# Performance work log

Hardware: AMD Instinct MI355X
Metric: run time of the kernel (lower is better)

Reference implementation:

```python
import jax, jax.numpy as jnp
import numpy as np

# Gemma2-9B layer config
HID = 3584
H = 16          # query heads
KV = 8          # kv heads
G = H // KV     # GQA group size
DH = 256        # head dim
INTER = 14336
WINDOW = 1024   # sliding window size
LOGIT_CAP = 50.0
SCALING = 256.0 ** -0.5   # query_pre_attn_scalar ** -0.5
EPS = 1e-6
ROPE_BASE = 10000.0
B, S = 2, 2048


def gemma_rmsnorm(x, w, eps=EPS):
    # Gemma RMSNorm: fp32 compute, scale by (1 + w)
    xf = x.astype(jnp.float32)
    var = jnp.mean(xf * xf, axis=-1, keepdims=True)
    return (xf * jax.lax.rsqrt(var + eps) * (1.0 + w.astype(jnp.float32))).astype(x.dtype)


def apply_rope(pos, x):
    # neox-style rotary embedding; x: [B, S, n_heads, DH], pos: [B, S]
    half = DH // 2
    inv_freq = 1.0 / (ROPE_BASE ** (jnp.arange(0, half, dtype=jnp.float32) / half * 1.0))
    inv_freq = 1.0 / (ROPE_BASE ** (jnp.arange(0, DH, 2, dtype=jnp.float32) / DH))
    ang = pos.astype(jnp.float32)[..., None] * inv_freq          # [B, S, half]
    cos = jnp.cos(ang)[:, :, None, :]                            # [B, S, 1, half]
    sin = jnp.sin(ang)[:, :, None, :]
    x1, x2 = x[..., :half], x[..., half:]
    return jnp.concatenate([x1 * cos - x2 * sin, x2 * cos + x1 * sin], axis=-1).astype(x.dtype)


def setup_inputs() -> dict:
    key = jax.random.key(0)
    ks = jax.random.split(key, 12)
    s = 0.02
    inp = {
        "hidden_states": jax.random.normal(ks[0], (B, S, HID), dtype=jnp.float32),
        "positions": jnp.tile(jnp.arange(S, dtype=jnp.int32)[None, :], (B, 1)),
        "in_ln_w": jax.random.normal(ks[1], (HID,), dtype=jnp.float32) * s,
        "post_attn_ln_w": jax.random.normal(ks[2], (HID,), dtype=jnp.float32) * s,
        "pre_ff_ln_w": jax.random.normal(ks[3], (HID,), dtype=jnp.float32) * s,
        "post_ff_ln_w": jax.random.normal(ks[4], (HID,), dtype=jnp.float32) * s,
        "q_w": jax.random.normal(ks[5], (HID, H * DH), dtype=jnp.float32) * s,
        "k_w": jax.random.normal(ks[6], (HID, KV * DH), dtype=jnp.float32) * s,
        "v_w": jax.random.normal(ks[7], (HID, KV * DH), dtype=jnp.float32) * s,
        "o_w": jax.random.normal(ks[8], (H * DH, HID), dtype=jnp.float32) * s,
        "gate_w": jax.random.normal(ks[9], (HID, INTER), dtype=jnp.float32) * s,
        "up_w": jax.random.normal(ks[10], (HID, INTER), dtype=jnp.float32) * s,
        "down_w": jax.random.normal(ks[11], (INTER, HID), dtype=jnp.float32) * s,
    }
    return inp


def _decoder_layer(hidden_states, positions, in_ln_w, post_attn_ln_w, pre_ff_ln_w,
                   post_ff_ln_w, q_w, k_w, v_w, o_w, gate_w, up_w, down_w):
    # residual is None path
    residual = hidden_states
    x = gemma_rmsnorm(hidden_states, in_ln_w)

    # ---- attention ----
    q = (x @ q_w).reshape(B, S, H, DH)
    k = (x @ k_w).reshape(B, S, KV, DH)
    v = (x @ v_w).reshape(B, S, KV, DH)
    q = apply_rope(positions, q)
    k = apply_rope(positions, k)
    kv_fused = jnp.stack([k, v], axis=0)  # paged KV-cache write, modeled densely

    qg = q.reshape(B, S, KV, G, DH)
    # scores: [B, KV, G, S(q), S(k)]
    scores = jnp.einsum('bsngd,btnd->bngst', qg, k) * SCALING
    scores = LOGIT_CAP * jnp.tanh(scores / LOGIT_CAP)  # logit softcapping
    i = jnp.arange(S)[:, None]
    j = jnp.arange(S)[None, :]
    mask = (j <= i) & (i - j < WINDOW)                 # causal + sliding window
    scores = jnp.where(mask, scores, jnp.finfo(scores.dtype).min)
    probs = jax.nn.softmax(scores, axis=-1)
    attn = jnp.einsum('bngst,btnd->bsngd', probs, v).reshape(B, S, H * DH)
    attn_out = attn @ o_w

    x = gemma_rmsnorm(attn_out, post_attn_ln_w)
    x = residual + x
    residual = x

    # ---- GeGLU MLP ----
    x = gemma_rmsnorm(x, pre_ff_ln_w)
    inter = (x @ up_w) * jax.nn.gelu(x @ gate_w)
    x = inter @ down_w
    x = gemma_rmsnorm(x, post_ff_ln_w)
    return x, residual, kv_fused


def reference(hidden_states, positions, in_ln_w, post_attn_ln_w, pre_ff_ln_w,
              post_ff_ln_w, q_w, k_w, v_w, o_w, gate_w, up_w, down_w):
    return _decoder_layer(hidden_states, positions, in_ln_w, post_attn_ln_w,
                          pre_ff_ln_w, post_ff_ln_w, q_w, k_w, v_w, o_w,
                          gate_w, up_w, down_w)
```

## Files before the change

kernel.cpp:

```cpp
#include <hip/hip_runtime.h>
#include <stdint.h>

typedef unsigned short ushortT;
typedef float f32x4 __attribute__((ext_vector_type(4)));
typedef short short8 __attribute__((ext_vector_type(8)));

#define HID 3584
#define NH 16
#define NKV 8
#define DH 256
#define SEQ 2048
#define NB 2
#define NTOK 4096
#define INTERDIM 14336
#define ICH 7168
#define WINDOW 1024

__device__ __forceinline__ ushortT f2bf(float x) {
  union { float f; uint32_t u; } v; v.f = x;
  uint32_t r = v.u + 0x7fffu + ((v.u >> 16) & 1u);
  return (ushortT)(r >> 16);
}
__device__ __forceinline__ float bf2f(uint32_t b) {
  union { uint32_t u; float f; } v; v.u = b << 16;
  return v.f;
}
__device__ __forceinline__ void gll16(const void* g, void* l) {
  __builtin_amdgcn_global_load_lds((const __attribute__((address_space(1))) void*)g,
                                   (__attribute__((address_space(3))) void*)l, 16, 0, 0);
}
__device__ __forceinline__ void sbar() {
  asm volatile("" ::: "memory");
  __builtin_amdgcn_s_barrier();
  asm volatile("" ::: "memory");
}
__device__ __forceinline__ void vmdrain() {
  asm volatile("s_waitcnt vmcnt(0)" ::: "memory");
}

__global__ __launch_bounds__(256) void transpose_cvt(const float* __restrict__ in,
                                                     ushortT* __restrict__ out,
                                                     int in_rs, int out_rs) {
  __shared__ float tile[64][65];
  const int r0 = blockIdx.y * 64, c0 = blockIdx.x * 64;
  const int t = threadIdx.x, tc = (t & 15) * 4, tr = t >> 4;
#pragma unroll
  for (int p = 0; p < 4; ++p) {
    int r = tr + p * 16;
    float4 v = *(const float4*)&in[(size_t)(r0 + r) * in_rs + c0 + tc];
    tile[r][tc] = v.x; tile[r][tc + 1] = v.y; tile[r][tc + 2] = v.z; tile[r][tc + 3] = v.w;
  }
  __syncthreads();
#pragma unroll
  for (int p = 0; p < 4; ++p) {
    int r = tr + p * 16;
    ushort4 u;
    u.x = f2bf(tile[tc + 0][r]); u.y = f2bf(tile[tc + 1][r]);
    u.z = f2bf(tile[tc + 2][r]); u.w = f2bf(tile[tc + 3][r]);
    *(ushort4*)&out[(size_t)(c0 + r) * out_rs + r0 + tc] = u;
  }
}

__global__ __launch_bounds__(256) void vtrans(const float* __restrict__ vsrc,
                                              ushortT* __restrict__ vT) {
  __shared__ float tile[64][65];
  const int z = blockIdx.z, b = z >> 3, n = z & 7;
  const float* in = vsrc + (size_t)b * SEQ * (NKV * DH) + n * DH;
  ushortT* out = vT + (size_t)z * DH * SEQ;
  const int s0 = blockIdx.y * 64, d0 = blockIdx.x * 64;
  const int t = threadIdx.x, tc = (t & 15) * 4, tr = t >> 4;
#pragma unroll
  for (int p = 0; p < 4; ++p) {
    int r = tr + p * 16;
    float4 v = *(const float4*)&in[(size_t)(s0 + r) * (NKV * DH) + d0 + tc];
    tile[r][tc] = v.x; tile[r][tc + 1] = v.y; tile[r][tc + 2] = v.z; tile[r][tc + 3] = v.w;
  }
  __syncthreads();
#pragma unroll
  for (int p = 0; p < 4; ++p) {
    int r = tr + p * 16;
    ushort4 u;
    u.x = f2bf(tile[tc + 0][r]); u.y = f2bf(tile[tc + 1][r]);
    u.z = f2bf(tile[tc + 2][r]); u.w = f2bf(tile[tc + 3][r]);
    *(ushort4*)&out[(size_t)(d0 + r) * SEQ + s0 + tc] = u;
  }
}

__device__ __forceinline__ float block_sum448(float v, float* sb) {
#pragma unroll
  for (int o = 32; o; o >>= 1) v += __shfl_xor(v, o, 64);
  __syncthreads();
  if ((threadIdx.x & 63) == 0) sb[threadIdx.x >> 6] = v;
  __syncthreads();
  float s = 0.f;
#pragma unroll
  for (int i = 0; i < 7; ++i) s += sb[i];
  return s;
}

__global__ __launch_bounds__(448) void rms_in(const float* __restrict__ in,
                                              const float* __restrict__ w,
                                              ushortT* __restrict__ out) {
  __shared__ float sb[8];
  const size_t row = blockIdx.x;
  const int c = threadIdx.x * 8;
  const float* p = in + row * HID + c;
  float4 a = *(const float4*)p, bq = *(const float4*)(p + 4);
  float v[8] = {a.x, a.y, a.z, a.w, bq.x, bq.y, bq.z, bq.w};
  float ssq = 0.f;
#pragma unroll
  for (int j = 0; j < 8; ++j) ssq += v[j] * v[j];
  float s = block_sum448(ssq, sb);
  float rs = rsqrtf(s * (1.0f / HID) + 1e-6f);
  uint32_t o[4];
#pragma unroll
  for (int j = 0; j < 4; ++j) {
    float r0 = v[2 * j] * rs * (1.f + w[c + 2 * j]);
    float r1 = v[2 * j + 1] * rs * (1.f + w[c + 2 * j + 1]);
    o[j] = (uint32_t)f2bf(r0) | ((uint32_t)f2bf(r1) << 16);
  }
  *(uint4*)(out + row * HID + c) = make_uint4(o[0], o[1], o[2], o[3]);
}

__global__ __launch_bounds__(448) void rms_add(const float* ao,
                                               const float* __restrict__ h,
                                               const float* __restrict__ w1,
                                               const float* __restrict__ w2,
                                               float* resid,
                                               ushortT* __restrict__ x2) {
  __shared__ float sb[8];
  const size_t row = blockIdx.x;
  const int c = threadIdx.x * 8;
  const float* p = ao + row * HID + c;
  float4 a = *(const float4*)p, bq = *(const float4*)(p + 4);
  float v[8] = {a.x, a.y, a.z, a.w, bq.x, bq.y, bq.z, bq.w};
  float ssq = 0.f;
#pragma unroll
  for (int j = 0; j < 8; ++j) ssq += v[j] * v[j];
  float s1 = block_sum448(ssq, sb);
  float rs1 = rsqrtf(s1 * (1.0f / HID) + 1e-6f);
  const float* hp = h + row * HID + c;
  float4 h0 = *(const float4*)hp, h1 = *(const float4*)(hp + 4);
  float hv[8] = {h0.x, h0.y, h0.z, h0.w, h1.x, h1.y, h1.z, h1.w};
  float r[8];
  float ssq2 = 0.f;
#pragma unroll
  for (int j = 0; j < 8; ++j) {
    r[j] = hv[j] + v[j] * rs1 * (1.f + w1[c + j]);
    ssq2 += r[j] * r[j];
  }
  float* rp = resid + row * HID + c;
  *(float4*)rp = make_float4(r[0], r[1], r[2], r[3]);
  *(float4*)(rp + 4) = make_float4(r[4], r[5], r[6], r[7]);
  float s2 = block_sum448(ssq2, sb);
  float rs2 = rsqrtf(s2 * (1.0f / HID) + 1e-6f);
  uint32_t o[4];
#pragma unroll
  for (int j = 0; j < 4; ++j) {
    float q0 = r[2 * j] * rs2 * (1.f + w2[c + 2 * j]);
    float q1 = r[2 * j + 1] * rs2 * (1.f + w2[c + 2 * j + 1]);
    o[j] = (uint32_t)f2bf(q0) | ((uint32_t)f2bf(q1) << 16);
  }
  *(uint4*)(x2 + row * HID + c) = make_uint4(o[0], o[1], o[2], o[3]);
}

__global__ __launch_bounds__(448) void rms_out(const float* in,
                                               const float* __restrict__ w,
                                               float* out) {
  __shared__ float sb[8];
  const size_t row = blockIdx.x;
  const int c = threadIdx.x * 8;
  const float* p = in + row * HID + c;
  float4 a = *(const float4*)p, bq = *(const float4*)(p + 4);
  float v[8] = {a.x, a.y, a.z, a.w, bq.x, bq.y, bq.z, bq.w};
  float ssq = 0.f;
#pragma unroll
  for (int j = 0; j < 8; ++j) ssq += v[j] * v[j];
  float s = block_sum448(ssq, sb);
  float rs = rsqrtf(s * (1.0f / HID) + 1e-6f);
  float* op = out + row * HID + c;
  float r[8];
#pragma unroll
  for (int j = 0; j < 8; ++j) r[j] = v[j] * rs * (1.f + w[c + j]);
  *(float4*)op = make_float4(r[0], r[1], r[2], r[3]);
  *(float4*)(op + 4) = make_float4(r[4], r[5], r[6], r[7]);
}

__global__ __launch_bounds__(128) void rope_q_k(const ushortT* __restrict__ qraw,
                                                const int* __restrict__ pos,
                                                ushortT* __restrict__ qr) {
  const int s = blockIdx.x, h = blockIdx.y, b = blockIdx.z, i = threadIdx.x;
  float p = (float)pos[b * SEQ + s];
  float ang = p * exp2f(-(float)i * (13.287712379549449f / 128.f));
  float sn, cs;
  sincosf(ang, &sn, &cs);
  size_t ib = ((size_t)b * SEQ + s) * (NH * DH) + (size_t)h * DH + i;
  float x1 = bf2f(qraw[ib]), x2 = bf2f(qraw[ib + 128]);
  size_t ob = (((size_t)b * NH + h) * SEQ + s) * DH + i;
  qr[ob] = f2bf(x1 * cs - x2 * sn);
  qr[ob + 128] = f2bf(x2 * cs + x1 * sn);
}

__global__ __launch_bounds__(128) void rope_k_k(const ushortT* __restrict__ kraw,
                                                const int* __restrict__ pos,
                                                ushortT* __restrict__ kr,
                                                float* __restrict__ kv0) {
  const int s = blockIdx.x, n = blockIdx.y, b = blockIdx.z, i = threadIdx.x;
  float p = (float)pos[b * SEQ + s];
  float ang = p * exp2f(-(float)i * (13.287712379549449f / 128.f));
  float sn, cs;
  sincosf(ang, &sn, &cs);
  size_t ib = ((size_t)b * SEQ + s) * (NKV * DH) + (size_t)n * DH + i;
  float x1 = bf2f(kraw[ib]), x2 = bf2f(kraw[ib + 128]);
  float o1 = x1 * cs - x2 * sn, o2 = x2 * cs + x1 * sn;
  size_t ob = (((size_t)b * NKV + n) * SEQ + s) * DH + i;
  kr[ob] = f2bf(o1);
  kr[ob + 128] = f2bf(o2);
  size_t kb = (((size_t)b * SEQ + s) * NKV + n) * DH + i;
  kv0[kb] = o1;
  kv0[kb + 128] = o2;
}

template <int OUTMODE>
__global__ __launch_bounds__(512) void gemm256(const ushortT* __restrict__ A, int lda,
                                               const ushortT* __restrict__ Bt, int ldb,
                                               void* __restrict__ C, int N, int K) {
  __shared__ ushortT lds[65536];
  char* lbase = (char*)lds;
  const int tid = threadIdx.x;
  const int nwg = gridDim.x * gridDim.y;
  const int lin = blockIdx.y * gridDim.x + blockIdx.x;
  const int cpx = nwg >> 3;
  const int lin2 = (lin & 7) * cpx + (lin >> 3);
  const int bx = lin2 % gridDim.x, by = lin2 / gridDim.x;
  const int m0 = by * 256, n0 = bx * 256;
  const int l = tid & 63, lr = l & 15, lg = l >> 4;
  const int wid = tid >> 6, wm2 = wid >> 2, wn4 = wid & 3;
  const int sr = tid >> 3, sc = tid & 7;

  f32x4 acc[8][4];
#pragma unroll
  for (int i = 0; i < 8; ++i)
#pragma unroll
    for (int j = 0; j < 4; ++j) acc[i][j] = (f32x4){0.f, 0.f, 0.f, 0.f};

  const int nt = K >> 6;
  const ushortT* Abase = A + (size_t)m0 * lda;
  const ushortT* Bbase = Bt + (size_t)n0 * ldb;

  auto stage_op = [&](const ushortT* gsrc, int ld, char* ldst) {
#pragma unroll
    for (int Li = 0; Li < 4; ++Li) {
      int r = Li * 64 + sr;
      gll16((const char*)(gsrc + (size_t)r * ld) + ((sc ^ (r & 7)) << 4),
            ldst + Li * 8192 + tid * 16);
    }
  };

  stage_op(Abase, lda, lbase);
  stage_op(Bbase, ldb, lbase + 32768);

  for (int t = 0; t < nt; ++t) {
    const int cur = t & 1, nxt = cur ^ 1;
    const char* Ab = lbase + cur * 65536 + wm2 * 16384;
    const char* Bb = lbase + cur * 65536 + 32768 + (wn4 >> 1) * 16384;
    short8 af[4][2], bfr[2][2];
#pragma unroll
    for (int q = 0; q < 4; ++q) {
      const int mh = q >> 1, nh = q & 1;
      if (q == 0) vmdrain();
      sbar();
      if (nh == 0) {
#pragma unroll
        for (int i = 0; i < 4; ++i) {
          int rA = mh * 64 + i * 16 + lr;
          int sw = rA & 7;
#pragma unroll
          for (int ks = 0; ks < 2; ++ks)
            af[i][ks] = *(const short8*)(Ab + rA * 128 + (((ks * 4 + lg) ^ sw) << 4));
        }
      }
#pragma unroll
      for (int j = 0; j < 2; ++j) {
        int rB = (wn4 & 1) * 64 + nh * 32 + j * 16 + lr;
        int sw = rB & 7;
#pragma unroll
        for (int ks = 0; ks < 2; ++ks)
          bfr[j][ks] = *(const short8*)(Bb + rB * 128 + (((ks * 4 + lg) ^ sw) << 4));
      }
      if (q == 0 && t + 1 < nt)
        stage_op(Abase + (size_t)(t + 1) * 64, lda, lbase + nxt * 65536);
      if (q == 1 && t + 1 < nt)
        stage_op(Bbase + (size_t)(t + 1) * 64, ldb, lbase + nxt * 65536 + 32768);
      __builtin_amdgcn_s_setprio(1);
#pragma unroll
      for (int i = 0; i < 4; ++i)
#pragma unroll
        for (int j = 0; j < 2; ++j)
#pragma unroll
          for (int ks = 0; ks < 2; ++ks)
            acc[mh * 4 + i][nh * 2 + j] = __builtin_amdgcn_mfma_f32_16x16x32_bf16(
                af[i][ks], bfr[j][ks], acc[mh * 4 + i][nh * 2 + j], 0, 0, 0);
      __builtin_amdgcn_s_setprio(0);
    }
  }
#pragma unroll
  for (int mi = 0; mi < 8; ++mi)
#pragma unroll
    for (int nj = 0; nj < 4; ++nj)
#pragma unroll
      for (int r = 0; r < 4; ++r) {
        size_t row = (size_t)(m0 + wm2 * 128 + mi * 16 + lg * 4 + r);
        size_t col = (size_t)(n0 + wn4 * 64 + nj * 16 + lr);
        if (OUTMODE == 0)
          ((float*)C)[row * N + col] = acc[mi][nj][r];
        else if (OUTMODE == 1)
          ((ushortT*)C)[row * N + col] = f2bf(acc[mi][nj][r]);
        else
          ((float*)C)[row * N + col] += acc[mi][nj][r];
      }
}

__global__ __launch_bounds__(256) void swiglu_k(const ushortT* __restrict__ g,
                                                const ushortT* __restrict__ u,
                                                ushortT* __restrict__ o, int n16) {
  int i = blockIdx.x * 256 + threadIdx.x;
  if (i >= n16) return;
  uint4 gv = ((const uint4*)g)[i];
  uint4 uv = ((const uint4*)u)[i];
  uint32_t ga[4] = {gv.x, gv.y, gv.z, gv.w};
  uint32_t ua[4] = {uv.x, uv.y, uv.z, uv.w};
  uint32_t rr[4];
#pragma unroll
  for (int j = 0; j < 4; ++j) {
    float g0 = bf2f(ga[j] & 0xffffu), g1 = bf2f(ga[j] >> 16);
    float u0 = bf2f(ua[j] & 0xffffu), u1 = bf2f(ua[j] >> 16);
    float e0 = 0.5f * g0 * (1.f + tanhf(0.7978845608f * (g0 + 0.044715f * g0 * g0 * g0)));
    float e1 = 0.5f * g1 * (1.f + tanhf(0.7978845608f * (g1 + 0.044715f * g1 * g1 * g1)));
    rr[j] = (uint32_t)f2bf(u0 * e0) | ((uint32_t)f2bf(u1 * e1) << 16);
  }
  ((uint4*)o)[i] = make_uint4(rr[0], rr[1], rr[2], rr[3]);
}

__global__ __launch_bounds__(256) void attn_fwd(const ushortT* __restrict__ Q,
                                                const ushortT* __restrict__ Kk,
                                                const ushortT* __restrict__ Vt,
                                                ushortT* __restrict__ Out) {
  __shared__ ushortT Kl[32 * 256];
  __shared__ ushortT Vl[256 * 32];
  __shared__ ushortT Pl[4][16 * 32];
  const int tid = threadIdx.x;
  const int w = tid >> 6, l = tid & 63, lr = l & 15, lg = l >> 4;
  const int h = blockIdx.y, b = blockIdx.z;
  const int n = h >> 1;
  const int qs = blockIdx.x * 64;
  const int sw = qs + w * 16;

  const ushortT* qp = Q + (((size_t)b * NH + h) * SEQ + (sw + lr)) * DH;
  short8 qf[8];
#pragma unroll
  for (int kk = 0; kk < 8; ++kk) qf[kk] = *(const short8*)(qp + kk * 32 + lg * 8);

  f32x4 acc[16];
#pragma unroll
  for (int i = 0; i < 16; ++i) acc[i] = (f32x4){0.f, 0.f, 0.f, 0.f};
  float m_s = -1e30f, l_s = 0.f;

  const ushortT* Kbase = Kk + ((size_t)b * NKV + n) * SEQ * DH;
  const ushortT* Vbase = Vt + ((size_t)b * NKV + n) * DH * SEQ;

  int tlo = qs - (WINDOW - 1);
  if (tlo < 0) tlo = 0;
  const int t0b = tlo & ~31;
  const int nt = (qs + 64 - t0b) >> 5;
  const int scol = sw + lr;

  for (int it = 0; it < nt; ++it) {
    const int t0 = t0b + it * 32;
    __syncthreads();
    {
      const int rowk = tid >> 5;
      const int cbk = (tid & 31) * 16;
#pragma unroll
      for (int c = 0; c < 4; ++c) {
        int row = c * 8 + rowk;
        int cbs = cbk ^ ((row & 7) << 4);
        gll16((const char*)(Kbase + (size_t)(t0 + row) * DH) + cbs, (char*)Kl + c * 4096 + tid * 16);
      }
      const int rowv = tid >> 2;
      const int cbv = (tid & 3) * 16;
#pragma unroll
      for (int c = 0; c < 4; ++c) {
        int row = c * 64 + rowv;
        int cbs = cbv ^ ((row & 3) << 4);
        gll16((const char*)(Vbase + (size_t)row * SEQ + t0) + cbs, (char*)Vl + c * 4096 + tid * 16);
      }
    }
    __syncthreads();
    f32x4 st[2];
#pragma unroll
    for (int tt = 0; tt < 2; ++tt) {
      f32x4 a = (f32x4){0.f, 0.f, 0.f, 0.f};
      const int krow = tt * 16 + lr;
      const char* kb = (const char*)Kl + krow * 512;
      const int swz = (krow & 7) << 4;
#pragma unroll
      for (int kk = 0; kk < 8; ++kk) {
        short8 kf = *(const short8*)(kb + ((kk * 64 + lg * 16) ^ swz));
        a = __builtin_amdgcn_mfma_f32_16x16x32_bf16(kf, qf[kk], a, 0, 0, 0);
      }
      st[tt] = a;
    }
    float pvv[8];
    float tmax = -1e30f;
#pragma unroll
    for (int tt = 0; tt < 2; ++tt)
#pragma unroll
      for (int r = 0; r < 4; ++r) {
        int t = t0 + tt * 16 + lg * 4 + r;
        float x = st[tt][r] * 0.0625f;
        x = 50.f * tanhf(x * 0.02f);
        bool ok = (t <= scol) && (scol - t < WINDOW);
        x = ok ? x : -1e30f;
        pvv[tt * 4 + r] = x;
        tmax = fmaxf(tmax, x);
      }
    tmax = fmaxf(tmax, __shfl_xor(tmax, 16, 64));
    tmax = fmaxf(tmax, __shfl_xor(tmax, 32, 64));
    float mnew = fmaxf(m_s, tmax);
    float fsc = __expf(m_s - mnew);
    m_s = mnew;
    float tsum = 0.f;
#pragma unroll
    for (int i = 0; i < 8; ++i) {
      pvv[i] = __expf(pvv[i] - mnew);
      tsum += pvv[i];
    }
    tsum += __shfl_xor(tsum, 16, 64);
    tsum += __shfl_xor(tsum, 32, 64);
    l_s = l_s * fsc + tsum;
    {
      char* pb = (char*)&Pl[w][0] + lr * 64;
      const int pswz = (lr & 3) << 4;
#pragma unroll
      for (int tt = 0; tt < 2; ++tt) {
        uint32_t p01 = (uint32_t)f2bf(pvv[tt * 4 + 0]) | ((uint32_t)f2bf(pvv[tt * 4 + 1]) << 16);
        uint32_t p23 = (uint32_t)f2bf(pvv[tt * 4 + 2]) | ((uint32_t)f2bf(pvv[tt * 4 + 3]) << 16);
        *(uint32_t*)(pb + ((tt * 32 + lg * 8 + 0) ^ pswz)) = p01;
        *(uint32_t*)(pb + ((tt * 32 + lg * 8 + 4) ^ pswz)) = p23;
      }
    }
    float fr[4];
#pragma unroll
    for (int r = 0; r < 4; ++r) fr[r] = __shfl(fsc, lg * 4 + r, 64);
#pragma unroll
    for (int nd = 0; nd < 16; ++nd) {
      acc[nd][0] *= fr[0]; acc[nd][1] *= fr[1];
      acc[nd][2] *= fr[2]; acc[nd][3] *= fr[3];
    }
    const char* pfb = (const char*)&Pl[w][0] + lr * 64;
    short8 pf = *(const short8*)(pfb + ((lg * 16) ^ ((lr & 3) << 4)));
#pragma unroll
    for (int nd = 0; nd < 16; ++nd) {
      const int vrow = nd * 16 + lr;
      short8 vf = *(const short8*)((const char*)Vl + vrow * 64 + ((lg * 16) ^ ((vrow & 3) << 4)));
      acc[nd] = __builtin_amdgcn_mfma_f32_16x16x32_bf16(pf, vf, acc[nd], 0, 0, 0);
    }
  }
  float linv[4];
#pragma unroll
  for (int r = 0; r < 4; ++r) linv[r] = 1.f / __shfl(l_s, lg * 4 + r, 64);
#pragma unroll
  for (int nd = 0; nd < 16; ++nd)
#pragma unroll
    for (int r = 0; r < 4; ++r) {
      size_t row = (size_t)b * SEQ + sw + lg * 4 + r;
      Out[row * (NH * DH) + (size_t)h * DH + nd * 16 + lr] = f2bf(acc[nd][r] * linv[r]);
    }
}

extern "C" void kernel_launch(void* const* d_in, const int* in_sizes, int n_in,
                              void* d_out, int out_size, void* d_ws, size_t ws_size,
                              hipStream_t stream) {
  const float* hs = (const float*)d_in[0];
  const int* pos = (const int*)d_in[1];
  const float* w_in = (const float*)d_in[2];
  const float* w_pa = (const float*)d_in[3];
  const float* w_pf = (const float*)d_in[4];
  const float* w_po = (const float*)d_in[5];
  const float* qw = (const float*)d_in[6];
  const float* kw = (const float*)d_in[7];
  const float* vw = (const float*)d_in[8];
  const float* ow = (const float*)d_in[9];
  const float* gw = (const float*)d_in[10];
  const float* uw = (const float*)d_in[11];
  const float* dw = (const float*)d_in[12];

  float* out_x = (float*)d_out;
  float* out_res = out_x + (size_t)NTOK * HID;
  float* out_kv0 = out_res + (size_t)NTOK * HID;
  float* out_kv1 = out_kv0 + (size_t)NTOK * NKV * DH;

  char* ws = (char*)d_ws;
  char* W = ws;
  ushortT* qwT = (ushortT*)(W);
  ushortT* kwT = (ushortT*)(W + 29360128);
  ushortT* vwT = (ushortT*)(W + 29360128 + 14680064);
  ushortT* owT = (ushortT*)(W + 29360128 + 2 * 14680064);
  ushortT* wS0 = (ushortT*)(W);
  ushortT* wS1 = (ushortT*)(W + 51380224);
  char* R = ws + 102760448;
  ushortT* x1 = (ushortT*)(R);
  ushortT* qraw_b = (ushortT*)(R + 29360128);
  ushortT* kraw_b = (ushortT*)(R + 62914560);
  ushortT* qrope = (ushortT*)(R + 79691776);
  ushortT* krope = (ushortT*)(R + 113246208);
  ushortT* vT = (ushortT*)(R + 130023424);
  ushortT* attnb = qraw_b;
  ushortT* x2 = x1;
  ushortT* gateC = (ushortT*)(R + 29360128);
  ushortT* upC = (ushortT*)(R + 29360128 + 58720256);
  ushortT* interC = gateC;
  float* attn_out = out_res;

  transpose_cvt<<<dim3(4096 / 64, HID / 64), 256, 0, stream>>>(qw, qwT, 4096, HID);
  transpose_cvt<<<dim3(2048 / 64, HID / 64), 256, 0, stream>>>(kw, kwT, 2048, HID);
  transpose_cvt<<<dim3(2048 / 64, HID / 64), 256, 0, stream>>>(vw, vwT, 2048, HID);
  transpose_cvt<<<dim3(HID / 64, 4096 / 64), 256, 0, stream>>>(ow, owT, HID, 4096);

  rms_in<<<NTOK, 448, 0, stream>>>(hs, w_in, x1);

  gemm256<1><<<dim3(16, 16), 512, 0, stream>>>(x1, HID, qwT, HID, qraw_b, 4096, HID);
  gemm256<1><<<dim3(8, 16), 512, 0, stream>>>(x1, HID, kwT, HID, kraw_b, 2048, HID);
  gemm256<0><<<dim3(8, 16), 512, 0, stream>>>(x1, HID, vwT, HID, out_kv1, 2048, HID);

  rope_q_k<<<dim3(SEQ, NH, NB), 128, 0, stream>>>(qraw_b, pos, qrope);
  rope_k_k<<<dim3(SEQ, NKV, NB), 128, 0, stream>>>(kraw_b, pos, krope, out_kv0);
  vtrans<<<dim3(DH / 64, SEQ / 64, NB * NKV), 256, 0, stream>>>(out_kv1, vT);

  attn_fwd<<<dim3(SEQ / 64, NH, NB), 256, 0, stream>>>(qrope, krope, vT, attnb);

  gemm256<0><<<dim3(HID / 256, 16), 512, 0, stream>>>(attnb, 4096, owT, 4096, attn_out, HID, 4096);

  rms_add<<<NTOK, 448, 0, stream>>>(attn_out, hs, w_pa, w_pf, out_res, x2);

  for (int c = 0; c < 2; ++c) {
    transpose_cvt<<<dim3(ICH / 64, HID / 64), 256, 0, stream>>>(gw + (size_t)c * ICH, wS0,
                                                                INTERDIM, HID);
    gemm256<1><<<dim3(ICH / 256, 16), 512, 0, stream>>>(x2, HID, wS0, HID, gateC, ICH, HID);
    transpose_cvt<<<dim3(ICH / 64, HID / 64), 256, 0, stream>>>(uw + (size_t)c * ICH, wS1,
                                                                INTERDIM, HID);
    gemm256<1><<<dim3(ICH / 256, 16), 512, 0, stream>>>(x2, HID, wS1, HID, upC, ICH, HID);
    int n16 = (int)((size_t)NTOK * ICH / 8);
    swiglu_k<<<(n16 + 255) / 256, 256, 0, stream>>>(gateC, upC, interC, n16);
    transpose_cvt<<<dim3(HID / 64, ICH / 64), 256, 0, stream>>>(dw + (size_t)c * ICH * HID, wS0,
                                                                HID, ICH);
    if (c == 0)
      gemm256<0><<<dim3(HID / 256, 16), 512, 0, stream>>>(interC, ICH, wS0, ICH, out_x, HID, ICH);
    else
      gemm256<2><<<dim3(HID / 256, 16), 512, 0, stream>>>(interC, ICH, wS0, ICH, out_x, HID, ICH);
  }

  rms_out<<<NTOK, 448, 0, stream>>>(out_x, w_po, out_x);
}
```

Baseline: 2.187 ms.

## Fuse QK projections, fold GELU gating into up-GEMM epilogue, unchunk MLP

The Q and K projections become one GEMM with N=6144 over the contiguous transposed weights. The rope kernels now read from a shared interleaved QK buffer. The MLP no longer runs in two intermediate chunks, so each of the gate, up and down GEMMs runs once over the full intermediate dimension. A new epilogue mode in the up GEMM applies the tanh-GELU of the gate value and the multiply in place, which removes the separate elementwise kernel and the accumulate-into-output pass of the down GEMM. This trades fewer launches and less intermediate memory traffic for a larger workspace footprint and a gate buffer that is read and overwritten in place.

```diff
diff --git a/kernel.cpp b/kernel.cpp
--- a/kernel.cpp
+++ b/kernel.cpp
@@ -13,7 +13,6 @@
 #define NB 2
 #define NTOK 4096
 #define INTERDIM 14336
-#define ICH 7168
 #define WINDOW 1024
 
 __device__ __forceinline__ ushortT f2bf(float x) {
@@ -186,7 +185,7 @@
   *(float4*)(op + 4) = make_float4(r[4], r[5], r[6], r[7]);
 }
 
-__global__ __launch_bounds__(128) void rope_q_k(const ushortT* __restrict__ qraw,
+__global__ __launch_bounds__(128) void rope_q_k(const ushortT* __restrict__ qk,
                                                 const int* __restrict__ pos,
                                                 ushortT* __restrict__ qr) {
   const int s = blockIdx.x, h = blockIdx.y, b = blockIdx.z, i = threadIdx.x;
@@ -194,14 +193,14 @@
   float ang = p * exp2f(-(float)i * (13.287712379549449f / 128.f));
   float sn, cs;
   sincosf(ang, &sn, &cs);
-  size_t ib = ((size_t)b * SEQ + s) * (NH * DH) + (size_t)h * DH + i;
-  float x1 = bf2f(qraw[ib]), x2 = bf2f(qraw[ib + 128]);
+  size_t ib = ((size_t)b * SEQ + s) * 6144 + (size_t)h * DH + i;
+  float x1 = bf2f(qk[ib]), x2 = bf2f(qk[ib + 128]);
   size_t ob = (((size_t)b * NH + h) * SEQ + s) * DH + i;
   qr[ob] = f2bf(x1 * cs - x2 * sn);
   qr[ob + 128] = f2bf(x2 * cs + x1 * sn);
 }
 
-__global__ __launch_bounds__(128) void rope_k_k(const ushortT* __restrict__ kraw,
+__global__ __launch_bounds__(128) void rope_k_k(const ushortT* __restrict__ qk,
                                                 const int* __restrict__ pos,
                                                 ushortT* __restrict__ kr,
                                                 float* __restrict__ kv0) {
@@ -210,8 +209,8 @@
   float ang = p * exp2f(-(float)i * (13.287712379549449f / 128.f));
   float sn, cs;
   sincosf(ang, &sn, &cs);
-  size_t ib = ((size_t)b * SEQ + s) * (NKV * DH) + (size_t)n * DH + i;
-  float x1 = bf2f(kraw[ib]), x2 = bf2f(kraw[ib + 128]);
+  size_t ib = ((size_t)b * SEQ + s) * 6144 + 4096 + (size_t)n * DH + i;
+  float x1 = bf2f(qk[ib]), x2 = bf2f(qk[ib + 128]);
   float o1 = x1 * cs - x2 * sn, o2 = x2 * cs + x1 * sn;
   size_t ob = (((size_t)b * NKV + n) * SEQ + s) * DH + i;
   kr[ob] = f2bf(o1);
@@ -224,7 +223,8 @@
 template <int OUTMODE>
 __global__ __launch_bounds__(512) void gemm256(const ushortT* __restrict__ A, int lda,
                                                const ushortT* __restrict__ Bt, int ldb,
-                                               void* __restrict__ C, int N, int K) {
+                                               void* C, const ushortT* G,
+                                               int N, int K) {
   __shared__ ushortT lds[65536];
   char* lbase = (char*)lds;
   const int tid = threadIdx.x;
@@ -261,9 +261,9 @@
   stage_op(Bbase, ldb, lbase + 32768);
 
   for (int t = 0; t < nt; ++t) {
-    const int cur = t & 1, nxt = cur ^ 1;
-    const char* Ab = lbase + cur * 65536 + wm2 * 16384;
-    const char* Bb = lbase + cur * 65536 + 32768 + (wn4 >> 1) * 16384;
+    const int buf = t & 1;
+    const char* Ab = lbase + buf * 65536 + wm2 * 16384;
+    const char* Bb = lbase + buf * 65536 + 32768 + (wn4 >> 1) * 16384;
     short8 af[4][2], bfr[2][2];
 #pragma unroll
     for (int q = 0; q < 4; ++q) {
@@ -289,9 +289,9 @@
           bfr[j][ks] = *(const short8*)(Bb + rB * 128 + (((ks * 4 + lg) ^ sw) << 4));
       }
       if (q == 0 && t + 1 < nt)
-        stage_op(Abase + (size_t)(t + 1) * 64, lda, lbase + nxt * 65536);
+        stage_op(Abase + (size_t)(t + 1) * 64, lda, lbase + (buf ^ 1) * 65536);
       if (q == 1 && t + 1 < nt)
-        stage_op(Bbase + (size_t)(t + 1) * 64, ldb, lbase + nxt * 65536 + 32768);
+        stage_op(Bbase + (size_t)(t + 1) * 64, ldb, lbase + (buf ^ 1) * 65536 + 32768);
       __builtin_amdgcn_s_setprio(1);
 #pragma unroll
       for (int i = 0; i < 4; ++i)
@@ -312,34 +312,20 @@
       for (int r = 0; r < 4; ++r) {
         size_t row = (size_t)(m0 + wm2 * 128 + mi * 16 + lg * 4 + r);
         size_t col = (size_t)(n0 + wn4 * 64 + nj * 16 + lr);
+        size_t idx = row * N + col;
         if (OUTMODE == 0)
-          ((float*)C)[row * N + col] = acc[mi][nj][r];
+          ((float*)C)[idx] = acc[mi][nj][r];
         else if (OUTMODE == 1)
-          ((ushortT*)C)[row * N + col] = f2bf(acc[mi][nj][r]);
-        else
-          ((float*)C)[row * N + col] += acc[mi][nj][r];
-      }
-}
-
-__global__ __launch_bounds__(256) void swiglu_k(const ushortT* __restrict__ g,
-                                                const ushortT* __restrict__ u,
-                                                ushortT* __restrict__ o, int n16) {
-  int i = blockIdx.x * 256 + threadIdx.x;
-  if (i >= n16) return;
-  uint4 gv = ((const uint4*)g)[i];
-  uint4 uv = ((const uint4*)u)[i];
-  uint32_t ga[4] = {gv.x, gv.y, gv.z, gv.w};
-  uint32_t ua[4] = {uv.x, uv.y, uv.z, uv.w};
-  uint32_t rr[4];
-#pragma unroll
-  for (int j = 0; j < 4; ++j) {
-    float g0 = bf2f(ga[j] & 0xffffu), g1 = bf2f(ga[j] >> 16);
-    float u0 = bf2f(ua[j] & 0xffffu), u1 = bf2f(ua[j] >> 16);
-    float e0 = 0.5f * g0 * (1.f + tanhf(0.7978845608f * (g0 + 0.044715f * g0 * g0 * g0)));
-    float e1 = 0.5f * g1 * (1.f + tanhf(0.7978845608f * (g1 + 0.044715f * g1 * g1 * g1)));
-    rr[j] = (uint32_t)f2bf(u0 * e0) | ((uint32_t)f2bf(u1 * e1) << 16);
-  }
-  ((uint4*)o)[i] = make_uint4(rr[0], rr[1], rr[2], rr[3]);
+          ((ushortT*)C)[idx] = f2bf(acc[mi][nj][r]);
+        else if (OUTMODE == 2)
+          ((float*)C)[idx] += acc[mi][nj][r];
+        else {
+          float u = acc[mi][nj][r];
+          float g = bf2f(G[idx]);
+          float e = 0.5f * g * (1.f + tanhf(0.7978845608f * (g + 0.044715f * g * g * g)));
+          ((ushortT*)C)[idx] = f2bf(u * e);
+        }
+      }
 }
 
 __global__ __launch_bounds__(256) void attn_fwd(const ushortT* __restrict__ Q,
@@ -507,20 +493,17 @@
   ushortT* kwT = (ushortT*)(W + 29360128);
   ushortT* vwT = (ushortT*)(W + 29360128 + 14680064);
   ushortT* owT = (ushortT*)(W + 29360128 + 2 * 14680064);
-  ushortT* wS0 = (ushortT*)(W);
-  ushortT* wS1 = (ushortT*)(W + 51380224);
+  ushortT* wF = (ushortT*)(W);
   char* R = ws + 102760448;
   ushortT* x1 = (ushortT*)(R);
-  ushortT* qraw_b = (ushortT*)(R + 29360128);
-  ushortT* kraw_b = (ushortT*)(R + 62914560);
+  ushortT* qk_b = (ushortT*)(R + 29360128);
   ushortT* qrope = (ushortT*)(R + 79691776);
   ushortT* krope = (ushortT*)(R + 113246208);
   ushortT* vT = (ushortT*)(R + 130023424);
-  ushortT* attnb = qraw_b;
+  ushortT* attnb = qk_b;
   ushortT* x2 = x1;
-  ushortT* gateC = (ushortT*)(R + 29360128);
-  ushortT* upC = (ushortT*)(R + 29360128 + 58720256);
-  ushortT* interC = gateC;
+  ushortT* gateF = (ushortT*)(R + 29360128);
+  ushortT* interF = gateF;
   float* attn_out = out_res;
 
   transpose_cvt<<<dim3(4096 / 64, HID / 64), 256, 0, stream>>>(qw, qwT, 4096, HID);
@@ -530,36 +513,29 @@
 
   rms_in<<<NTOK, 448, 0, stream>>>(hs, w_in, x1);
 
-  gemm256<1><<<dim3(16, 16), 512, 0, stream>>>(x1, HID, qwT, HID, qraw_b, 4096, HID);
-  gemm256<1><<<dim3(8, 16), 512, 0, stream>>>(x1, HID, kwT, HID, kraw_b, 2048, HID);
-  gemm256<0><<<dim3(8, 16), 512, 0, stream>>>(x1, HID, vwT, HID, out_kv1, 2048, HID);
-
-  rope_q_k<<<dim3(SEQ, NH, NB), 128, 0, stream>>>(qraw_b, pos, qrope);
-  rope_k_k<<<dim3(SEQ, NKV, NB), 128, 0, stream>>>(kraw_b, pos, krope, out_kv0);
+  gemm256<1><<<dim3(24, 16), 512, 0, stream>>>(x1, HID, qwT, HID, qk_b, nullptr, 6144, HID);
+  gemm256<0><<<dim3(8, 16), 512, 0, stream>>>(x1, HID, vwT, HID, out_kv1, nullptr, 2048, HID);
+
+  rope_q_k<<<dim3(SEQ, NH, NB), 128, 0, stream>>>(qk_b, pos, qrope);
+  rope_k_k<<<dim3(SEQ, NKV, NB), 128, 0, stream>>>(qk_b, pos, krope, out_kv0);
   vtrans<<<dim3(DH / 64, SEQ / 64, NB * NKV), 256, 0, stream>>>(out_kv1, vT);
 
   attn_fwd<<<dim3(SEQ / 64, NH, NB), 256, 0, stream>>>(qrope, krope, vT, attnb);
 
-  gemm256<0><<<dim3(HID / 256, 16), 512, 0, stream>>>(attnb, 4096, owT, 4096, attn_out, HID, 4096);
+  gemm256<0><<<dim3(HID / 256, 16), 512, 0, stream>>>(attnb, 4096, owT, 4096, attn_out, nullptr,
+                                                      HID, 4096);
 
   rms_add<<<NTOK, 448, 0, stream>>>(attn_out, hs, w_pa, w_pf, out_res, x2);
 
-  for (int c = 0; c < 2; ++c) {
-    transpose_cvt<<<dim3(ICH / 64, HID / 64), 256, 0, stream>>>(gw + (size_t)c * ICH, wS0,
-                                                                INTERDIM, HID);
-    gemm256<1><<<dim3(ICH / 256, 16), 512, 0, stream>>>(x2, HID, wS0, HID, gateC, ICH, HID);
-    transpose_cvt<<<dim3(ICH / 64, HID / 64), 256, 0, stream>>>(uw + (size_t)c * ICH, wS1,
-                                                                INTERDIM, HID);
-    gemm256<1><<<dim3(ICH / 256, 16), 512, 0, stream>>>(x2, HID, wS1, HID, upC, ICH, HID);
-    int n16 = (int)((size_t)NTOK * ICH / 8);
-    swiglu_k<<<(n16 + 255) / 256, 256, 0, stream>>>(gateC, upC, interC, n16);
-    transpose_cvt<<<dim3(HID / 64, ICH / 64), 256, 0, stream>>>(dw + (size_t)c * ICH * HID, wS0,
-                                                                HID, ICH);
-    if (c == 0)
-      gemm256<0><<<dim3(HID / 256, 16), 512, 0, stream>>>(interC, ICH, wS0, ICH, out_x, HID, ICH);
-    else
-      gemm256<2><<<dim3(HID / 256, 16), 512, 0, stream>>>(interC, ICH, wS0, ICH, out_x, HID, ICH);
-  }
+  transpose_cvt<<<dim3(INTERDIM / 64, HID / 64), 256, 0, stream>>>(gw, wF, INTERDIM, HID);
+  gemm256<1><<<dim3(INTERDIM / 256, 16), 512, 0, stream>>>(x2, HID, wF, HID, gateF, nullptr,
+                                                           INTERDIM, HID);
+  transpose_cvt<<<dim3(INTERDIM / 64, HID / 64), 256, 0, stream>>>(uw, wF, INTERDIM, HID);
+  gemm256<3><<<dim3(INTERDIM / 256, 16), 512, 0, stream>>>(x2, HID, wF, HID, interF, gateF,
+                                                           INTERDIM, HID);
+  transpose_cvt<<<dim3(HID / 64, INTERDIM / 64), 256, 0, stream>>>(dw, wF, HID, INTERDIM);
+  gemm256<0><<<dim3(HID / 256, 16), 512, 0, stream>>>(interF, INTERDIM, wF, INTERDIM, out_x,
+                                                      nullptr, HID, INTERDIM);
 
   rms_out<<<NTOK, 448, 0, stream>>>(out_x, w_po, out_x);
 }
```

After: 2.233 ms. 1.02x slower.
